# Performance work log

Measured on AMD Instinct MI355X. Metric: run time of the kernel, lower is better.

The kernel has to match this reference:

```python
import jax, jax.numpy as jnp
import numpy as np

B, T, C, H = 4, 2048, 1024, 16
D = C // H  # head_dim = 64


def setup_inputs() -> dict:
    key = jax.random.key(0)
    k1, k2, k3 = jax.random.split(key, 3)
    x = jax.random.normal(k1, (B, T, C), dtype=jnp.float32)
    # nn.Linear weights: [out_features, in_features]
    W_attn = jax.random.normal(k2, (3 * C, C), dtype=jnp.float32) * (1.0 / np.sqrt(C))
    W_proj = jax.random.normal(k3, (C, C), dtype=jnp.float32) * (1.0 / np.sqrt(C))
    b_proj = jnp.zeros((C,), dtype=jnp.float32)
    return {"x": x, "W_attn": W_attn, "W_proj": W_proj, "b_proj": b_proj}


def reference(x, W_attn, W_proj, b_proj):
    Bx, Tx, Cx = x.shape
    # fused QKV projection (no bias), then split
    qkv = jnp.einsum('btc,oc->bto', x, W_attn)            # [B,T,3C]
    q, k, v = jnp.split(qkv, 3, axis=-1)                  # each [B,T,C]
    # [B,T,C] -> [B,H,T,D]
    def heads(t):
        return t.reshape(Bx, Tx, H, D).transpose(0, 2, 1, 3)
    q, k, v = heads(q), heads(k), heads(v)
    scale = 1.0 / np.sqrt(D).astype(np.float32)
    att = jnp.einsum('bhqd,bhkd->bhqk', q, k) * scale     # [B,H,T,T], no causal mask
    att = jax.nn.softmax(att, axis=-1)
    y = jnp.einsum('bhqk,bhkd->bhqd', att, v)             # [B,H,T,D]
    y = y.transpose(0, 2, 1, 3).reshape(Bx, Tx, Cx)       # [B,T,C]
    out = jnp.einsum('btc,oc->bto', y, W_proj) + b_proj   # output projection
    return out
```

## Files before the change

kernel.cpp:

```cpp
#include <hip/hip_runtime.h>


typedef _Float16 f16x8 __attribute__((ext_vector_type(8)));
typedef _Float16 f16x4 __attribute__((ext_vector_type(4)));
typedef _Float16 f16x2 __attribute__((ext_vector_type(2)));
typedef float f32x4 __attribute__((ext_vector_type(4)));

__device__ __forceinline__ void gl_lds16(const _Float16* g, _Float16* l) {
  __builtin_amdgcn_global_load_lds(
      (const __attribute__((address_space(1))) void*)g,
      (__attribute__((address_space(3))) void*)l, 16, 0, 0);
}

__global__ __launch_bounds__(256) void cvt_f32_f16(const float* __restrict__ src,
                                                   _Float16* __restrict__ dst, int n) {
  int i = (blockIdx.x * 256 + threadIdx.x) * 8;
  int stride = gridDim.x * 256 * 8;
  for (; i < n; i += stride) {
    float4 a = *(const float4*)(src + i);
    float4 b = *(const float4*)(src + i + 4);
    f16x8 o = {(_Float16)a.x, (_Float16)a.y, (_Float16)a.z, (_Float16)a.w,
               (_Float16)b.x, (_Float16)b.y, (_Float16)b.z, (_Float16)b.w};
    *(f16x8*)(dst + i) = o;
  }
}

template <bool BIAS, bool OUT_F16>
__global__ __launch_bounds__(256)
void gemm_bt(const _Float16* __restrict__ A, const _Float16* __restrict__ B,
             void* __restrict__ C, const float* __restrict__ bias,
             int M, int N, int K) {
  __shared__ _Float16 sA[128 * 32];
  __shared__ _Float16 sB[128 * 32];
  const int tid = threadIdx.x;
  const int w = tid >> 6, l = tid & 63, l15 = l & 15, l4 = l >> 4;
  const int wm = w >> 1, wn = w & 1;
  const size_t m0 = (size_t)blockIdx.y * 128, n0 = (size_t)blockIdx.x * 128;

  f32x4 acc[4][4] = {};

  const int sr = tid >> 2, sc = (tid & 3) * 8;
  const _Float16* aSrc = A + (m0 + sr) * (size_t)K + sc;
  const _Float16* bSrc = B + (n0 + sr) * (size_t)K + sc;
  _Float16* aDst = sA + tid * 8;
  _Float16* bDst = sB + tid * 8;
  const int K64 = 64 * K;

  for (int k0 = 0; k0 < K; k0 += 32) {
    __syncthreads();
    gl_lds16(aSrc + k0, aDst);
    gl_lds16(aSrc + K64 + k0, aDst + 2048);
    gl_lds16(bSrc + k0, bDst);
    gl_lds16(bSrc + K64 + k0, bDst + 2048);
    __syncthreads();
    f16x8 af[4], bf[4];
#pragma unroll
    for (int i = 0; i < 4; ++i) {
      af[i] = *(const f16x8*)(sA + (wm * 64 + i * 16 + l15) * 32 + l4 * 8);
      bf[i] = *(const f16x8*)(sB + (wn * 64 + i * 16 + l15) * 32 + l4 * 8);
    }
#pragma unroll
    for (int i = 0; i < 4; ++i)
#pragma unroll
      for (int j = 0; j < 4; ++j)
        acc[i][j] = __builtin_amdgcn_mfma_f32_16x16x32_f16(af[i], bf[j], acc[i][j], 0, 0, 0);
  }

#pragma unroll
  for (int i = 0; i < 4; ++i)
#pragma unroll
    for (int j = 0; j < 4; ++j) {
      size_t row = m0 + wm * 64 + i * 16 + l4 * 4;
      size_t col = n0 + wn * 64 + j * 16 + l15;
      float bv = 0.0f;
      if (BIAS) bv = bias[col];
#pragma unroll
      for (int rr = 0; rr < 4; ++rr) {
        float v = acc[i][j][rr] + bv;
        if (OUT_F16)
          ((_Float16*)C)[(row + rr) * N + col] = (_Float16)v;
        else
          ((float*)C)[(row + rr) * N + col] = v;
      }
    }
}

__global__ __launch_bounds__(256, 4)
void attn_kernel(const _Float16* __restrict__ qkv, _Float16* __restrict__ y16) {
  const int qt = blockIdx.x, bh = blockIdx.y;
  const int b = bh >> 4, h = bh & 15;
  const int tid = threadIdx.x;
  const int w = tid >> 6, l = tid & 63, l15 = l & 15, l4 = l >> 4;

  __shared__ _Float16 sK[128 * 64];
  __shared__ _Float16 sVt[64][136];

  const size_t rowbase = (size_t)b * 2048;
  const int qcol = h * 64, kcol = 1024 + h * 64, vcol = 2048 + h * 64;

  f16x8 bq[2][2];
  {
    const _Float16 csf = (_Float16)(0.125f * 1.44269504f);
#pragma unroll
    for (int qs = 0; qs < 2; ++qs) {
      size_t qrow = rowbase + qt * 128 + w * 32 + qs * 16 + l15;
#pragma unroll
      for (int ks = 0; ks < 2; ++ks) {
        f16x8 v = *(const f16x8*)(qkv + qrow * 3072 + qcol + ks * 32 + l4 * 8);
#pragma unroll
        for (int e = 0; e < 8; ++e) v[e] *= csf;
        bq[qs][ks] = v;
      }
    }
  }

  f32x4 accy[2][4] = {};
  f32x4 accl[2] = {};

  const _Float16 one0 = (l15 == 0) ? (_Float16)1.0f : (_Float16)0.0f;
  const f16x4 bv1 = {one0, one0, one0, one0};

  const int krow = w * 8 + (l >> 3);
  const int csrc = (l & 7) ^ (l >> 3);
  const _Float16* kSrc0 = qkv + (rowbase + krow) * 3072 + kcol + csrc * 8;
  _Float16* kDst0 = sK + w * 8 * 64 + l * 8;

  const int vrow = 2 * l, vd0 = w * 16;
  const _Float16* vSrc0 = qkv + (rowbase + vrow) * 3072 + vcol + vd0;

  f16x8 va0 = *(const f16x8*)(vSrc0);
  f16x8 va1 = *(const f16x8*)(vSrc0 + 8);
  f16x8 vb0 = *(const f16x8*)(vSrc0 + 3072);
  f16x8 vb1 = *(const f16x8*)(vSrc0 + 3072 + 8);

  for (int kb = 0; kb < 16; ++kb) {
    __syncthreads();
    {
      const _Float16* ks_ = kSrc0 + (size_t)kb * 128 * 3072;
#pragma unroll
      for (int j = 0; j < 4; ++j) gl_lds16(ks_ + (size_t)j * 32 * 3072, kDst0 + j * 2048);
#pragma unroll
      for (int e = 0; e < 8; ++e) {
        f16x2 p0; p0[0] = va0[e]; p0[1] = vb0[e];
        *(f16x2*)(&sVt[vd0 + e][vrow]) = p0;
        f16x2 p1; p1[0] = va1[e]; p1[1] = vb1[e];
        *(f16x2*)(&sVt[vd0 + 8 + e][vrow]) = p1;
      }
    }
    __syncthreads();

    if (kb + 1 < 16) {
      const _Float16* vs_ = vSrc0 + (size_t)(kb + 1) * 128 * 3072;
      va0 = *(const f16x8*)(vs_);
      va1 = *(const f16x8*)(vs_ + 8);
      vb0 = *(const f16x8*)(vs_ + 3072);
      vb1 = *(const f16x8*)(vs_ + 3072 + 8);
    }

#pragma unroll
    for (int sub = 0; sub < 2; ++sub) {
      f32x4 st[2][4] = {};
      __builtin_amdgcn_s_setprio(1);
#pragma unroll
      for (int m = 0; m < 4; ++m) {
        const int row = sub * 64 + m * 16 + l15;
#pragma unroll
        for (int ks = 0; ks < 2; ++ks) {
          const int cs_ = (ks * 4 + l4) ^ (l15 & 7);
          f16x8 ak = *(const f16x8*)(sK + row * 64 + cs_ * 8);
          st[0][m] = __builtin_amdgcn_mfma_f32_16x16x32_f16(ak, bq[0][ks], st[0][m], 0, 0, 0);
          st[1][m] = __builtin_amdgcn_mfma_f32_16x16x32_f16(ak, bq[1][ks], st[1][m], 0, 0, 0);
        }
      }
      __builtin_amdgcn_s_setprio(0);

      f16x4 pa[2][4];
#pragma unroll
      for (int qs = 0; qs < 2; ++qs) {
#pragma unroll
        for (int m = 0; m < 4; ++m) {
          float p0 = exp2f(st[qs][m][0]);
          float p1 = exp2f(st[qs][m][1]);
          float p2 = exp2f(st[qs][m][2]);
          float p3 = exp2f(st[qs][m][3]);
#if __has_builtin(__builtin_amdgcn_cvt_pkrtz)
          auto lo = __builtin_amdgcn_cvt_pkrtz(p0, p1);
          auto hi = __builtin_amdgcn_cvt_pkrtz(p2, p3);
          f16x4 pv;
          pv[0] = lo[0]; pv[1] = lo[1]; pv[2] = hi[0]; pv[3] = hi[1];
          pa[qs][m] = pv;
#else
          f16x4 pv;
          pv[0] = (_Float16)p0; pv[1] = (_Float16)p1;
          pv[2] = (_Float16)p2; pv[3] = (_Float16)p3;
          pa[qs][m] = pv;
#endif
        }
      }

      __builtin_amdgcn_s_setprio(1);
#pragma unroll
      for (int m = 0; m < 4; ++m) {
        const int kc = sub * 64 + m * 16 + l4 * 4;
        accl[0] = __builtin_amdgcn_mfma_f32_16x16x16f16(bv1, pa[0][m], accl[0], 0, 0, 0);
        accl[1] = __builtin_amdgcn_mfma_f32_16x16x16f16(bv1, pa[1][m], accl[1], 0, 0, 0);
#pragma unroll
        for (int dt = 0; dt < 4; ++dt) {
          f16x4 bv = *(const f16x4*)(&sVt[dt * 16 + l15][kc]);
          accy[0][dt] = __builtin_amdgcn_mfma_f32_16x16x16f16(bv, pa[0][m], accy[0][dt], 0, 0, 0);
          accy[1][dt] = __builtin_amdgcn_mfma_f32_16x16x16f16(bv, pa[1][m], accy[1][dt], 0, 0, 0);
        }
      }
      __builtin_amdgcn_s_setprio(0);
    }
  }

#pragma unroll
  for (int qs = 0; qs < 2; ++qs) {
    const float lsum = __shfl(accl[qs][0], l15);
    const float rinv = 1.0f / lsum;
    const size_t row = rowbase + qt * 128 + w * 32 + qs * 16 + l15;
#pragma unroll
    for (int dt = 0; dt < 4; ++dt) {
      f16x4 ov;
#pragma unroll
      for (int r = 0; r < 4; ++r) ov[r] = (_Float16)(accy[qs][dt][r] * rinv);
      *(f16x4*)(y16 + row * 1024 + h * 64 + dt * 16 + l4 * 4) = ov;
    }
  }
}

extern "C" void kernel_launch(void* const* d_in, const int* in_sizes, int n_in,
                              void* d_out, int out_size, void* d_ws, size_t ws_size,
                              hipStream_t stream) {
  (void)in_sizes; (void)n_in; (void)out_size; (void)ws_size;
  const float* x  = (const float*)d_in[0];
  const float* Wa = (const float*)d_in[1];
  const float* Wp = (const float*)d_in[2];
  const float* bp = (const float*)d_in[3];
  float* out = (float*)d_out;

  char* ws = (char*)d_ws;
  _Float16* x16   = (_Float16*)ws; ws += (size_t)8192 * 1024 * 2;
  _Float16* Wa16  = (_Float16*)ws; ws += (size_t)3072 * 1024 * 2;
  _Float16* Wp16  = (_Float16*)ws; ws += (size_t)1024 * 1024 * 2;
  _Float16* qkv16 = (_Float16*)ws; ws += (size_t)8192 * 3072 * 2;
  _Float16* y16   = (_Float16*)ws; ws += (size_t)8192 * 1024 * 2;

  cvt_f32_f16<<<4096, 256, 0, stream>>>(x, x16, 8192 * 1024);
  cvt_f32_f16<<<1536, 256, 0, stream>>>(Wa, Wa16, 3072 * 1024);
  cvt_f32_f16<<<512, 256, 0, stream>>>(Wp, Wp16, 1024 * 1024);

  gemm_bt<false, true><<<dim3(24, 64), 256, 0, stream>>>(x16, Wa16, (void*)qkv16, nullptr,
                                                         8192, 3072, 1024);
  attn_kernel<<<dim3(16, 64), 256, 0, stream>>>(qkv16, y16);
  gemm_bt<true, false><<<dim3(8, 64), 256, 0, stream>>>(y16, Wp16, (void*)out, bp,
                                                        8192, 1024, 1024);
}
```

Before: 326.7 us.

## Widen GEMM K-tile with swizzled LDS, remap attention blocks per XCD, raw exp2

The GEMM K-step doubles from 32 to 64 and the LDS columns get an XOR swizzle, which halves the number of barriers per K and aims to cut LDS bank conflicts. The attention grid becomes 1D and is remapped so each XCD handles the query tiles of a fixed set of heads, so K/V reuse stays within one L2. The softmax exp2 switches to the hardware builtin, skipping libm's range handling. The LDS footprint per GEMM block doubles, and the raw exp2 loses denormal handling.

```diff
diff --git a/kernel.cpp b/kernel.cpp
--- a/kernel.cpp
+++ b/kernel.cpp
@@ -10,6 +10,14 @@
   __builtin_amdgcn_global_load_lds(
       (const __attribute__((address_space(1))) void*)g,
       (__attribute__((address_space(3))) void*)l, 16, 0, 0);
+}
+
+__device__ __forceinline__ float fexp2(float x) {
+#if __has_builtin(__builtin_amdgcn_exp2f)
+  return __builtin_amdgcn_exp2f(x);
+#else
+  return exp2f(x);
+#endif
 }
 
 __global__ __launch_bounds__(256) void cvt_f32_f16(const float* __restrict__ src,
@@ -30,8 +38,8 @@
 void gemm_bt(const _Float16* __restrict__ A, const _Float16* __restrict__ B,
              void* __restrict__ C, const float* __restrict__ bias,
              int M, int N, int K) {
-  __shared__ _Float16 sA[128 * 32];
-  __shared__ _Float16 sB[128 * 32];
+  __shared__ _Float16 sA[128 * 64];
+  __shared__ _Float16 sB[128 * 64];
   const int tid = threadIdx.x;
   const int w = tid >> 6, l = tid & 63, l15 = l & 15, l4 = l >> 4;
   const int wm = w >> 1, wn = w & 1;
@@ -39,31 +47,39 @@
 
   f32x4 acc[4][4] = {};
 
-  const int sr = tid >> 2, sc = (tid & 3) * 8;
-  const _Float16* aSrc = A + (m0 + sr) * (size_t)K + sc;
-  const _Float16* bSrc = B + (n0 + sr) * (size_t)K + sc;
+  const int sr = tid >> 3;
+  const int sc8 = (tid & 7) ^ ((tid >> 3) & 7);
+  const _Float16* aSrc = A + (m0 + sr) * (size_t)K + sc8 * 8;
+  const _Float16* bSrc = B + (n0 + sr) * (size_t)K + sc8 * 8;
   _Float16* aDst = sA + tid * 8;
   _Float16* bDst = sB + tid * 8;
-  const int K64 = 64 * K;
-
-  for (int k0 = 0; k0 < K; k0 += 32) {
-    __syncthreads();
-    gl_lds16(aSrc + k0, aDst);
-    gl_lds16(aSrc + K64 + k0, aDst + 2048);
-    gl_lds16(bSrc + k0, bDst);
-    gl_lds16(bSrc + K64 + k0, bDst + 2048);
-    __syncthreads();
-    f16x8 af[4], bf[4];
-#pragma unroll
-    for (int i = 0; i < 4; ++i) {
-      af[i] = *(const f16x8*)(sA + (wm * 64 + i * 16 + l15) * 32 + l4 * 8);
-      bf[i] = *(const f16x8*)(sB + (wn * 64 + i * 16 + l15) * 32 + l4 * 8);
-    }
-#pragma unroll
-    for (int i = 0; i < 4; ++i)
-#pragma unroll
-      for (int j = 0; j < 4; ++j)
-        acc[i][j] = __builtin_amdgcn_mfma_f32_16x16x32_f16(af[i], bf[j], acc[i][j], 0, 0, 0);
+  const size_t K32 = 32 * (size_t)K;
+
+  const int e7 = l15 & 7;
+
+  for (int k0 = 0; k0 < K; k0 += 64) {
+    __syncthreads();
+#pragma unroll
+    for (int j = 0; j < 4; ++j) {
+      gl_lds16(aSrc + j * K32 + k0, aDst + j * 2048);
+      gl_lds16(bSrc + j * K32 + k0, bDst + j * 2048);
+    }
+    __syncthreads();
+#pragma unroll
+    for (int ks = 0; ks < 2; ++ks) {
+      const int cs_ = ((ks * 4 + l4) ^ e7) * 8;
+      f16x8 af[4], bf[4];
+#pragma unroll
+      for (int i = 0; i < 4; ++i) {
+        af[i] = *(const f16x8*)(sA + (wm * 64 + i * 16 + l15) * 64 + cs_);
+        bf[i] = *(const f16x8*)(sB + (wn * 64 + i * 16 + l15) * 64 + cs_);
+      }
+#pragma unroll
+      for (int i = 0; i < 4; ++i)
+#pragma unroll
+        for (int j = 0; j < 4; ++j)
+          acc[i][j] = __builtin_amdgcn_mfma_f32_16x16x32_f16(af[i], bf[j], acc[i][j], 0, 0, 0);
+    }
   }
 
 #pragma unroll
@@ -87,7 +103,10 @@
 
 __global__ __launch_bounds__(256, 4)
 void attn_kernel(const _Float16* __restrict__ qkv, _Float16* __restrict__ y16) {
-  const int qt = blockIdx.x, bh = blockIdx.y;
+  const int lin = blockIdx.x;
+  const int xcd = lin & 7;
+  const int bh = xcd * 8 + (lin >> 7);
+  const int qt = (lin >> 3) & 15;
   const int b = bh >> 4, h = bh & 15;
   const int tid = threadIdx.x;
   const int w = tid >> 6, l = tid & 63, l15 = l & 15, l4 = l >> 4;
@@ -179,10 +198,10 @@
       for (int qs = 0; qs < 2; ++qs) {
 #pragma unroll
         for (int m = 0; m < 4; ++m) {
-          float p0 = exp2f(st[qs][m][0]);
-          float p1 = exp2f(st[qs][m][1]);
-          float p2 = exp2f(st[qs][m][2]);
-          float p3 = exp2f(st[qs][m][3]);
+          float p0 = fexp2(st[qs][m][0]);
+          float p1 = fexp2(st[qs][m][1]);
+          float p2 = fexp2(st[qs][m][2]);
+          float p3 = fexp2(st[qs][m][3]);
 #if __has_builtin(__builtin_amdgcn_cvt_pkrtz)
           auto lo = __builtin_amdgcn_cvt_pkrtz(p0, p1);
           auto hi = __builtin_amdgcn_cvt_pkrtz(p2, p3);
@@ -253,7 +272,7 @@
 
   gemm_bt<false, true><<<dim3(24, 64), 256, 0, stream>>>(x16, Wa16, (void*)qkv16, nullptr,
                                                          8192, 3072, 1024);
-  attn_kernel<<<dim3(16, 64), 256, 0, stream>>>(qkv16, y16);
+  attn_kernel<<<1024, 256, 0, stream>>>(qkv16, y16);
   gemm_bt<true, false><<<dim3(8, 64), 256, 0, stream>>>(y16, Wp16, (void*)out, bp,
                                                         8192, 1024, 1024);
 }
```

Measured after the change: 285.7 us. 12.6% less time.
